# Optimization experiments

Hardware: AMD Instinct MI355X
Metric: run time of the kernel (lower is better)

## Reference

```python
import jax, jax.numpy as jnp
import numpy as np

C_IN = 256
H = W = 64
B = 2


def _conv3x3(x, w, b):
    # x: (B,C,H,W), w: (Co,Ci,3,3) -> (B,Co,H,W), stride 1, pad 1
    y = jax.lax.conv_general_dilated(x, w, (1, 1), 'SAME',
                                     dimension_numbers=('NCHW', 'OIHW', 'NCHW'))
    return y + b[None, :, None, None]


def _deform_conv3x3(x, offset, w, b):
    """torchvision-style DeformConv2d, kernel 3x3, stride 1, pad 1, dilation 1.
    x: (B,C,H,W); offset: (B,18,H,W) laid out as (k, [dy,dx]) per kernel tap;
    w: (Co,C,3,3); b: (Co,)
    """
    Bx, C, Hx, Wx = x.shape
    Co = w.shape[0]
    off = offset.reshape(Bx, 9, 2, Hx, Wx)
    # kernel tap k = ky*3 + kx, relative positions in {-1,0,1}
    ky = (jnp.arange(9) // 3 - 1).astype(x.dtype)
    kx = (jnp.arange(9) % 3 - 1).astype(x.dtype)
    py = (jnp.arange(Hx, dtype=x.dtype)[None, None, :, None]
          + ky[None, :, None, None] + off[:, :, 0])          # (B,9,H,W)
    px = (jnp.arange(Wx, dtype=x.dtype)[None, None, None, :]
          + kx[None, :, None, None] + off[:, :, 1])          # (B,9,H,W)
    y0f = jnp.floor(py)
    x0f = jnp.floor(px)
    wy = py - y0f
    wx = px - x0f
    y0 = y0f.astype(jnp.int32)
    x0 = x0f.astype(jnp.int32)
    xf = x.reshape(Bx, C, Hx * Wx)

    def corner(yc, xc, wgt):
        valid = (yc >= 0) & (yc < Hx) & (xc >= 0) & (xc < Wx)
        idx = jnp.clip(yc, 0, Hx - 1) * Wx + jnp.clip(xc, 0, Wx - 1)  # (B,9,H,W)
        g = jax.vmap(lambda xb, ib: xb[:, ib])(xf, idx.reshape(Bx, -1))  # (B,C,9HW)
        g = g.reshape(Bx, C, 9, Hx, Wx)
        return g * (wgt * valid)[:, None]  # (B,C,9,H,W)

    s = (corner(y0, x0, (1 - wy) * (1 - wx))
         + corner(y0, x0 + 1, (1 - wy) * wx)
         + corner(y0 + 1, x0, wy * (1 - wx))
         + corner(y0 + 1, x0 + 1, wy * wx))
    out = jnp.einsum('ock,bckhw->bohw', w.reshape(Co, C, 9), s)
    return out + b[None, :, None, None]


def setup_inputs() -> dict:
    key = jax.random.key(0)
    ks = jax.random.split(key, 10)
    C8 = C_IN // 8
    sc = 0.02  # small init so offsets stay O(1) pixels
    return {
        'x': jax.random.normal(ks[0], (B, C_IN, H, W), jnp.float32),
        'w_off': jax.random.normal(ks[1], (18, C_IN, 3, 3), jnp.float32) * sc,
        'b_off': jnp.zeros((18,), jnp.float32),
        'wq': jax.random.normal(ks[2], (C8, C_IN, 3, 3), jnp.float32) * sc,
        'bq': jnp.zeros((C8,), jnp.float32),
        'wk': jax.random.normal(ks[3], (C8, C_IN, 3, 3), jnp.float32) * sc,
        'bk': jnp.zeros((C8,), jnp.float32),
        'wv': jax.random.normal(ks[4], (C_IN, C_IN, 3, 3), jnp.float32) * sc,
        'bv': jnp.zeros((C_IN,), jnp.float32),
        'gamma': jnp.full((1,), 0.5, jnp.float32),  # module inits to 0; nonzero for a non-trivial baseline
    }


def reference(x, w_off, b_off, wq, bq, wk, bk, wv, bv, gamma):
    Bx, C, Hx, Wx = x.shape
    HW = Hx * Wx
    offset = _conv3x3(x, w_off, b_off)                       # (B,18,H,W)
    q = _deform_conv3x3(x, offset, wq, bq).reshape(Bx, HW, -1)  # (B,HW,C//8)
    k = _deform_conv3x3(x, offset, wk, bk).reshape(Bx, HW, -1)  # (B,HW,C//8)
    v = _deform_conv3x3(x, offset, wv, bv).reshape(Bx, HW, -1)  # (B,HW,C)
    attn = jax.nn.softmax(jnp.einsum('bqc,bkc->bqk', q, k), axis=-1)  # (B,HW,HW)
    out = jnp.einsum('bqk,bkc->bqc', attn, v).reshape(Bx, C, Hx, Wx)
    return gamma * out + x
```

## Files before the change

### kernel.cpp

```cpp
#include <hip/hip_runtime.h>
#include <math.h>
#include <stdint.h>

#define CIN 256
#define HH 64
#define WW 64
#define HW 4096
#define CHW (CIN * HW)

typedef __attribute__((ext_vector_type(8))) short short8;
typedef __attribute__((ext_vector_type(4))) float float4v;

__device__ inline unsigned short f2bf(float f) {
    union { float f; uint32_t u; } v; v.f = f;
    return (unsigned short)((v.u + 0x7FFFu + ((v.u >> 16) & 1u)) >> 16);
}
__device__ inline float bf2f(unsigned short h) {
    union { uint32_t u; float f; } v; v.u = ((uint32_t)h) << 16;
    return v.f;
}
__device__ inline uint4 ld16(const unsigned short* p) {
    uint4 r; __builtin_memcpy(&r, p, 16); return r;
}

__global__ __launch_bounds__(256) void k_offset_conv(
    const float* __restrict__ x, const float* __restrict__ w_off,
    float* __restrict__ off_part)
{
    __shared__ float red[4][64][18];
    const int bh = blockIdx.x, cg = blockIdx.y;
    const int b = bh >> 6, h = bh & 63;
    const int t = threadIdx.x;
    const int w = t & 63;
    const int wv = __builtin_amdgcn_readfirstlane(t >> 6);
    float acc[18];
#pragma unroll
    for (int i = 0; i < 18; ++i) acc[i] = 0.f;
    const float* xb = x + (size_t)b * CHW;
#pragma unroll
    for (int ci = 0; ci < 8; ++ci) {
        const int c = cg * 32 + wv * 8 + ci;
        const float* xc = xb + (size_t)c * HW;
        float r0 = (h > 0)  ? xc[(h - 1) * WW + w] : 0.f;
        float r1 =            xc[h * WW + w];
        float r2 = (h < 63) ? xc[(h + 1) * WW + w] : 0.f;
        float l0 = __shfl_up(r0, 1), l1 = __shfl_up(r1, 1), l2 = __shfl_up(r2, 1);
        float d0 = __shfl_down(r0, 1), d1 = __shfl_down(r1, 1), d2 = __shfl_down(r2, 1);
        if (w == 0)  { l0 = 0.f; l1 = 0.f; l2 = 0.f; }
        if (w == 63) { d0 = 0.f; d1 = 0.f; d2 = 0.f; }
        const float xv[9] = {l0, r0, d0, l1, r1, d1, l2, r2, d2};
        const float* wc = w_off + (size_t)c * 9;
#pragma unroll
        for (int co = 0; co < 18; ++co) {
            const float* wp = wc + (size_t)co * (CIN * 9);
#pragma unroll
            for (int k = 0; k < 9; ++k) acc[co] += wp[k] * xv[k];
        }
    }
#pragma unroll
    for (int co = 0; co < 18; ++co) red[wv][w][co] = acc[co];
    __syncthreads();
    if (t < 64) {
#pragma unroll
        for (int co = 0; co < 18; ++co) {
            float s = red[0][t][co] + red[1][t][co] + red[2][t][co] + red[3][t][co];
            off_part[((size_t)(cg * 128 + bh)) * 1152 + co * 64 + t] = s;
        }
    }
}

__global__ __launch_bounds__(256) void k_params(
    const float* __restrict__ off_part, const float* __restrict__ b_off,
    uint2* __restrict__ pbw, uint32_t* __restrict__ pba)
{
    const int bh = blockIdx.x;
    const int h = bh & 63;
    const int t = threadIdx.x;
    for (int r = 0; r < 3; ++r) {
        int sid = t + 256 * r;
        if (sid < 576) {
            int k = sid >> 6, ww = sid & 63;
            float dy = b_off[2 * k], dx = b_off[2 * k + 1];
#pragma unroll
            for (int g = 0; g < 8; ++g) {
                const float* pp = off_part + (size_t)(g * 128 + bh) * 1152;
                dy += pp[(2 * k) * 64 + ww];
                dx += pp[(2 * k + 1) * 64 + ww];
            }
            float py = (float)(h + k / 3 - 1) + dy;
            float px = (float)(ww + k % 3 - 1) + dx;
            float y0f = floorf(py), x0f = floorf(px);
            float fy = py - y0f, fx = px - x0f;
            int y0 = (int)y0f, x0 = (int)x0f;
            int yb = min(max(y0, 0), 62), xb = min(max(x0, 0), 62);
            float wr[2] = {0.f, 0.f}, wc[2] = {0.f, 0.f};
            if (y0 >= 0 && y0 < HH) wr[y0 - yb] += 1.f - fy;
            if (y0 + 1 >= 0 && y0 + 1 < HH) wr[y0 + 1 - yb] += fy;
            if (x0 >= 0 && x0 < WW) wc[x0 - xb] += 1.f - fx;
            if (x0 + 1 >= 0 && x0 + 1 < WW) wc[x0 + 1 - xb] += fx;
            uint2 pw;
            pw.x = (uint32_t)f2bf(wr[0] * wc[0]) | ((uint32_t)f2bf(wr[0] * wc[1]) << 16);
            pw.y = (uint32_t)f2bf(wr[1] * wc[0]) | ((uint32_t)f2bf(wr[1] * wc[1]) << 16);
            pbw[(size_t)bh * 576 + sid] = pw;
            pba[(size_t)bh * 576 + sid] = (uint32_t)(yb * WW + xb);
        }
    }
}

__global__ __launch_bounds__(256) void k_wcat(
    const float* __restrict__ wq, const float* __restrict__ wk, const float* __restrict__ wv_,
    const float* __restrict__ bq, const float* __restrict__ bk, const float* __restrict__ bv,
    unsigned short* __restrict__ wf, float* __restrict__ bcat)
{
    int e = (blockIdx.x * 256 + threadIdx.x) * 4;
    const float* src;
    if (e < 32 * 2304)      src = wq + e;
    else if (e < 64 * 2304) src = wk + (e - 32 * 2304);
    else                    src = wv_ + (e - 64 * 2304);
    float4 v = *(const float4*)src;
    unsigned short o[4] = {f2bf(v.x), f2bf(v.y), f2bf(v.z), f2bf(v.w)};
    int co = e / 2304;
    int k0 = e - co * 2304;
#pragma unroll
    for (int i = 0; i < 4; ++i) {
        int k = k0 + i;
        int c = (k * 7282) >> 16;
        int tap = k - c * 9;
        int kdp = tap * 256 + c;
        size_t d = ((size_t)(co >> 4) * 72 + (kdp >> 5)) * 512 + (size_t)(co & 15) * 32 + (kdp & 31);
        wf[d] = o[i];
    }
    if (blockIdx.x == 0 && threadIdx.x < 320) {
        int c = threadIdx.x;
        bcat[c] = c < 32 ? bq[c] : (c < 64 ? bk[c - 32] : bv[c - 64]);
    }
}

__global__ __launch_bounds__(256) void k_xt(
    const float* __restrict__ x, unsigned short* __restrict__ xt)
{
    __shared__ float tl[64][65];
    const int b = blockIdx.y, px0 = blockIdx.x * 64;
    const int t = threadIdx.x;
    const float* xb = x + (size_t)b * CHW;
    unsigned short* xo = xt + (size_t)b * CHW;
    for (int cb = 0; cb < 4; ++cb) {
        __syncthreads();
#pragma unroll
        for (int i = 0; i < 16; ++i) {
            int cr = (t >> 6) * 16 + i;
            tl[cr][t & 63] = xb[(size_t)(cb * 64 + cr) * HW + px0 + (t & 63)];
        }
        __syncthreads();
#pragma unroll
        for (int i = 0; i < 2; ++i) {
            int px = t >> 2;
            int sl = (t & 3) + 4 * i;
            union { uint4 v; unsigned short u[8]; } o;
#pragma unroll
            for (int j = 0; j < 8; ++j) o.u[j] = f2bf(tl[sl * 8 + j][px]);
            *(uint4*)(xo + (size_t)(px0 + px) * 256 + cb * 64 + sl * 8) = o.v;
        }
    }
}

__global__ __launch_bounds__(256) void k_dgemm(
    const unsigned short* __restrict__ xt, const uint2* __restrict__ pbw,
    const uint32_t* __restrict__ pba, const unsigned short* __restrict__ wf,
    const float* __restrict__ bcat,
    unsigned short* __restrict__ qb16, unsigned short* __restrict__ kb16,
    unsigned short* __restrict__ vb16)
{
    __shared__ uint2 prw2[144];
    __shared__ uint32_t pra2[144];
    __shared__ unsigned short tile[2][4][16][40];

    const int blk = blockIdx.x;
    const int b = blk >> 8;
    const int p0 = (blk & 255) * 16;
    const int bh = b * 64 + (p0 >> 6);
    const int w0 = p0 & 63;

    const int t = threadIdx.x;
    const int lane = t & 63;
    const int l15 = lane & 15, quad = lane >> 4;
    const int wvid = __builtin_amdgcn_readfirstlane(t >> 6);

    if (t < 144) {
        int nl9 = t / 9, tap = t - nl9 * 9;
        int src = bh * 576 + tap * 64 + w0 + nl9;
        prw2[nl9 * 9 + tap] = pbw[src];
        pra2[nl9 * 9 + tap] = pba[src];
    }

    const unsigned short* xtb = xt + (size_t)b * CHW;
    const int px = t >> 4;
    const int cl = (t >> 2) & 3;
    const int sl = t & 3;

    float4v acc[5];
#pragma unroll
    for (int s = 0; s < 5; ++s) acc[s] = (float4v){0.f, 0.f, 0.f, 0.f};

    const unsigned short* ap[5];
#pragma unroll
    for (int s = 0; s < 5; ++s)
        ap[s] = wf + (size_t)(s * 4 + wvid) * 72 * 512 + (size_t)l15 * 32 + quad * 8;

    __syncthreads();

    uint2 wcur; uint4 u00, u01, u10, u11;
    {
        int idx = px * 9 + 0;
        wcur = prw2[idx];
        const unsigned short* xp = xtb + (size_t)pra2[idx] * 256 + (0 + cl) * 32 + sl * 8;
        u00 = ld16(xp); u01 = ld16(xp + 256); u10 = ld16(xp + 16384); u11 = ld16(xp + 16640);
    }

#pragma unroll
    for (int m = 0; m < 18; ++m) {
        const int tap = m >> 1, q0 = (m & 1) * 4;

        float w00 = bf2f((unsigned short)(wcur.x & 0xFFFF));
        float w01 = bf2f((unsigned short)(wcur.x >> 16));
        float w10 = bf2f((unsigned short)(wcur.y & 0xFFFF));
        float w11 = bf2f((unsigned short)(wcur.y >> 16));
        union { uint4 v; unsigned short u[8]; } a00, a01, a10, a11, o;
        a00.v = u00; a01.v = u01; a10.v = u10; a11.v = u11;
#pragma unroll
        for (int j = 0; j < 8; ++j) {
            float v = w00 * bf2f(a00.u[j]) + w01 * bf2f(a01.u[j])
                    + w10 * bf2f(a10.u[j]) + w11 * bf2f(a11.u[j]);
            o.u[j] = f2bf(v);
        }

        if (m < 17) {
            int tapn = (m + 1) >> 1, q0n = ((m + 1) & 1) * 4;
            int idx = px * 9 + tapn;
            wcur = prw2[idx];
            const unsigned short* xp = xtb + (size_t)pra2[idx] * 256 + (q0n + cl) * 32 + sl * 8;
            u00 = ld16(xp); u01 = ld16(xp + 256); u10 = ld16(xp + 16384); u11 = ld16(xp + 16640);
        }

        *(uint4*)&tile[m & 1][cl][px][sl * 8] = o.v;
        asm volatile("s_waitcnt lgkmcnt(0)\n\ts_barrier" ::: "memory");

#pragma unroll
        for (int st = 0; st < 4; ++st) {
            const int kt = tap * 8 + q0 + st;
            short8 bfr = *(const short8*)&tile[m & 1][st][l15][quad * 8];
#pragma unroll
            for (int s = 0; s < 5; ++s) {
                uint4 a = *(const uint4*)(ap[s] + (size_t)kt * 512);
                acc[s] = __builtin_amdgcn_mfma_f32_16x16x32_bf16(*(const short8*)&a, bfr, acc[s], 0, 0, 0);
            }
        }
    }

#pragma unroll
    for (int s = 0; s < 5; ++s) {
        const int cobase = s * 64 + wvid * 16;
        unsigned short* ob; int lco; size_t nper;
        if (cobase < 32)      { ob = qb16; lco = cobase;      nper = (size_t)32 * HW; }
        else if (cobase < 64) { ob = kb16; lco = cobase - 32; nper = (size_t)32 * HW; }
        else                  { ob = vb16; lco = cobase - 64; nper = (size_t)256 * HW; }
        unsigned short* obb = ob + (size_t)b * nper;
#pragma unroll
        for (int r = 0; r < 4; ++r) {
            float val = acc[s][r] + bcat[cobase + (quad << 2) + r];
            obb[(size_t)(lco + (quad << 2) + r) * HW + p0 + l15] = f2bf(val);
        }
    }
}

__global__ __launch_bounds__(256) void k_vtrans(
    const unsigned short* __restrict__ vb16, unsigned short* __restrict__ vb16T)
{
    const int jt = blockIdx.x, b = blockIdx.y;
    const int cc = threadIdx.x;
    const unsigned short* src = vb16 + (size_t)b * CHW + (size_t)(jt * 64) * 256 + cc;
    unsigned short* dst = vb16T + (size_t)b * CHW + (size_t)cc * 4096 + jt * 64;
#pragma unroll
    for (int o = 0; o < 8; ++o) {
        union { uint4 v; unsigned short u[8]; } tmp;
#pragma unroll
        for (int j = 0; j < 8; ++j) tmp.u[j] = src[(o * 8 + j) * 256];
        *(uint4*)(dst + o * 8) = tmp.v;
    }
}

#define SM_SHIFT 16.0f
__global__ __launch_bounds__(256) void k_attn(
    const unsigned short* __restrict__ qb16, const unsigned short* __restrict__ kb16,
    const unsigned short* __restrict__ vt, const float* __restrict__ x,
    const float* __restrict__ gamma, float* __restrict__ out)
{
    __shared__ unsigned short ptl[4][16 * 40];
    __shared__ unsigned short Vt[2][64][40];
    __shared__ unsigned short Kt[2][32][36];
    __shared__ float red[2][64][20];

    const int qt = blockIdx.x, ch = blockIdx.y, b = blockIdx.z;
    const int t = threadIdx.x;
    const int lane = t & 63;
    const int wv = t >> 6;
    const int g = wv & 1, jh = wv >> 1;
    const int l15 = lane & 15, quad = lane >> 4;
    const int cc0 = ch * 64;

    const unsigned short* Qb = qb16 + (size_t)b * (32 * 4096);
    const unsigned short* Kb = kb16 + (size_t)b * (32 * 4096);
    const unsigned short* VT = vt + (size_t)b * CHW;

    const int q0 = qt * 32 + g * 16;
    short8 qfr = *(const short8*)(Qb + (size_t)(q0 + l15) * 32 + quad * 8);

    const int vcc = t >> 2, voff = (t & 3) * 8;
    const int ktile = t >> 7, ktl = t & 127;
    const int krow = ktl >> 2, koff = (ktl & 3) * 8;

    float l_i = 0.f;
    float4v acc[4];
#pragma unroll
    for (int s = 0; s < 4; ++s) acc[s] = (float4v){0.f, 0.f, 0.f, 0.f};
    unsigned short* pw = ptl[wv];

    for (int rnd = 0; rnd < 64; ++rnd) {
        const int j0a = rnd * 32;
        uint4 v0 = *(const uint4*)(VT + (size_t)(cc0 + vcc) * 4096 + j0a + voff);
        uint4 v1 = *(const uint4*)(VT + (size_t)(cc0 + vcc) * 4096 + 2048 + j0a + voff);
        uint4 kv = *(const uint4*)(Kb + (size_t)(ktile * 2048 + j0a + krow) * 32 + koff);
        __syncthreads();
        *(uint4*)&Vt[0][vcc][voff] = v0;
        *(uint4*)&Vt[1][vcc][voff] = v1;
        *(uint4*)&Kt[ktile][krow][koff] = kv;
        __syncthreads();
        short8 kfr0 = *(const short8*)&Kt[jh][l15][quad * 8];
        short8 kfr1 = *(const short8*)&Kt[jh][16 + l15][quad * 8];
        float4v s0 = (float4v){0.f, 0.f, 0.f, 0.f}, s1 = s0;
        s0 = __builtin_amdgcn_mfma_f32_16x16x32_bf16(kfr0, qfr, s0, 0, 0, 0);
        s1 = __builtin_amdgcn_mfma_f32_16x16x32_bf16(kfr1, qfr, s1, 0, 0, 0);
        float p[8]; float ls = 0.f;
#pragma unroll
        for (int r = 0; r < 4; ++r) { p[r] = __expf(s0[r] - SM_SHIFT); ls += p[r]; }
#pragma unroll
        for (int r = 0; r < 4; ++r) { p[4 + r] = __expf(s1[r] - SM_SHIFT); ls += p[4 + r]; }
        l_i += ls;
        union { uint2 v; unsigned short u[4]; } pk0, pk1;
#pragma unroll
        for (int r = 0; r < 4; ++r) { pk0.u[r] = f2bf(p[r]); pk1.u[r] = f2bf(p[4 + r]); }
        *(uint2*)&pw[l15 * 40 + (quad << 2)] = pk0.v;
        *(uint2*)&pw[l15 * 40 + 16 + (quad << 2)] = pk1.v;
        short8 pfr = *(const short8*)&pw[l15 * 40 + quad * 8];
#pragma unroll
        for (int s = 0; s < 4; ++s) {
            short8 vfr = *(const short8*)&Vt[jh][s * 16 + l15][quad * 8];
            acc[s] = __builtin_amdgcn_mfma_f32_16x16x32_bf16(pfr, vfr, acc[s], 0, 0, 0);
        }
    }

    l_i += __shfl_xor(l_i, 16);
    l_i += __shfl_xor(l_i, 32);

    __syncthreads();
    if (jh == 1) {
#pragma unroll
        for (int s = 0; s < 4; ++s) *(float4v*)&red[g][lane][s * 4] = acc[s];
        red[g][lane][16] = l_i;
    }
    __syncthreads();
    if (jh == 0) {
#pragma unroll
        for (int s = 0; s < 4; ++s) {
            float4v o = *(const float4v*)&red[g][lane][s * 4];
            acc[s][0] += o[0]; acc[s][1] += o[1]; acc[s][2] += o[2]; acc[s][3] += o[3];
        }
        l_i += red[g][lane][16];
        float lr[4];
#pragma unroll
        for (int r = 0; r < 4; ++r) lr[r] = __shfl(l_i, (quad << 2) + r);
        const float gm = gamma[0];
        const float* xb = x + (size_t)b * CHW;
        float* ob = out + (size_t)b * CHW;
#pragma unroll
        for (int s = 0; s < 4; ++s) {
#pragma unroll
            for (int r = 0; r < 4; ++r) {
                int q = q0 + (quad << 2) + r;
                int cc = cc0 + s * 16 + l15;
                size_t idx = (size_t)q * 256 + cc;
                ob[idx] = gm * (acc[s][r] / lr[r]) + xb[idx];
            }
        }
    }
}

extern "C" void kernel_launch(void* const* d_in, const int* in_sizes, int n_in,
                              void* d_out, int out_size, void* d_ws, size_t ws_size,
                              hipStream_t stream)
{
    (void)in_sizes; (void)n_in; (void)out_size; (void)ws_size;
    const float* x     = (const float*)d_in[0];
    const float* w_off = (const float*)d_in[1];
    const float* b_off = (const float*)d_in[2];
    const float* wq    = (const float*)d_in[3];
    const float* bq    = (const float*)d_in[4];
    const float* wk    = (const float*)d_in[5];
    const float* bk    = (const float*)d_in[6];
    const float* wv    = (const float*)d_in[7];
    const float* bv    = (const float*)d_in[8];
    const float* gamma = (const float*)d_in[9];
    float* out = (float*)d_out;

    char* ws = (char*)d_ws;
    uint2*          pbw     = (uint2*)(ws + 589824);
    uint32_t*       pba     = (uint32_t*)(ws + 1179648);
    unsigned short* qb16    = (unsigned short*)(ws + 1474560);
    unsigned short* kb16    = (unsigned short*)(ws + 1998848);
    unsigned short* vb16T   = (unsigned short*)(ws + 2523136);
    unsigned short* wfb     = (unsigned short*)(ws + 6717440);
    float*          bcat    = (float*)(ws + 8192000);
    float*          off_part = (float*)d_out;
    unsigned short* vb16     = (unsigned short*)d_out;
    unsigned short* xtb      = (unsigned short*)((char*)d_out + 4194304);

    k_offset_conv<<<dim3(128, 8), 256, 0, stream>>>(x, w_off, off_part);
    k_params<<<dim3(128), 256, 0, stream>>>(off_part, b_off, pbw, pba);
    k_wcat<<<dim3(720), 256, 0, stream>>>(wq, wk, wv, bq, bk, bv, wfb, bcat);
    k_xt<<<dim3(64, 2), 256, 0, stream>>>(x, xtb);
    k_dgemm<<<dim3(512), 256, 0, stream>>>(xtb, pbw, pba, wfb, bcat, qb16, kb16, vb16);
    k_vtrans<<<dim3(64, 2), 256, 0, stream>>>(vb16, vb16T);
    k_attn<<<dim3(128, 4, 2), 256, 0, stream>>>(qb16, kb16, vb16T, x, gamma, out);
}
```

Measured before the change: 260.7 us.

## Double queries per attention block and prefetch next K/V tile into registers

```diff
diff --git a/kernel.cpp b/kernel.cpp
--- a/kernel.cpp
+++ b/kernel.cpp
@@ -295,10 +295,10 @@
     const unsigned short* __restrict__ vt, const float* __restrict__ x,
     const float* __restrict__ gamma, float* __restrict__ out)
 {
-    __shared__ unsigned short ptl[4][16 * 40];
-    __shared__ unsigned short Vt[2][64][40];
+    __shared__ unsigned short ptl[8][16 * 40];
+    __shared__ unsigned short Vt[2][64][36];
     __shared__ unsigned short Kt[2][32][36];
-    __shared__ float red[2][64][20];
+    __shared__ float red[2][64][36];
 
     const int qt = blockIdx.x, ch = blockIdx.y, b = blockIdx.z;
     const int t = threadIdx.x;
@@ -312,84 +312,131 @@
     const unsigned short* Kb = kb16 + (size_t)b * (32 * 4096);
     const unsigned short* VT = vt + (size_t)b * CHW;
 
-    const int q0 = qt * 32 + g * 16;
-    short8 qfr = *(const short8*)(Qb + (size_t)(q0 + l15) * 32 + quad * 8);
+    const int qbase = qt * 64 + g * 32;
+    short8 qfr0 = *(const short8*)(Qb + (size_t)(qbase + l15) * 32 + quad * 8);
+    short8 qfr1 = *(const short8*)(Qb + (size_t)(qbase + 16 + l15) * 32 + quad * 8);
 
     const int vcc = t >> 2, voff = (t & 3) * 8;
     const int ktile = t >> 7, ktl = t & 127;
     const int krow = ktl >> 2, koff = (ktl & 3) * 8;
 
-    float l_i = 0.f;
-    float4v acc[4];
-#pragma unroll
-    for (int s = 0; s < 4; ++s) acc[s] = (float4v){0.f, 0.f, 0.f, 0.f};
-    unsigned short* pw = ptl[wv];
+    float l_i0 = 0.f, l_i1 = 0.f;
+    float4v acc[2][4];
+#pragma unroll
+    for (int u = 0; u < 2; ++u)
+#pragma unroll
+        for (int s = 0; s < 4; ++s) acc[u][s] = (float4v){0.f, 0.f, 0.f, 0.f};
+    unsigned short* pw0 = ptl[wv * 2];
+    unsigned short* pw1 = ptl[wv * 2 + 1];
+
+    uint4 v0, v1, kv;
+    {
+        const unsigned short* vp = VT + (size_t)(cc0 + vcc) * 4096 + voff;
+        v0 = ld16(vp);
+        v1 = ld16(vp + 2048);
+        kv = ld16(Kb + (size_t)(ktile * 2048 + krow) * 32 + koff);
+    }
 
     for (int rnd = 0; rnd < 64; ++rnd) {
-        const int j0a = rnd * 32;
-        uint4 v0 = *(const uint4*)(VT + (size_t)(cc0 + vcc) * 4096 + j0a + voff);
-        uint4 v1 = *(const uint4*)(VT + (size_t)(cc0 + vcc) * 4096 + 2048 + j0a + voff);
-        uint4 kv = *(const uint4*)(Kb + (size_t)(ktile * 2048 + j0a + krow) * 32 + koff);
-        __syncthreads();
+        asm volatile("s_waitcnt lgkmcnt(0)\n\ts_barrier" ::: "memory");
         *(uint4*)&Vt[0][vcc][voff] = v0;
         *(uint4*)&Vt[1][vcc][voff] = v1;
         *(uint4*)&Kt[ktile][krow][koff] = kv;
-        __syncthreads();
+        asm volatile("s_waitcnt lgkmcnt(0)\n\ts_barrier" ::: "memory");
+
+        if (rnd < 63) {
+            const int j0n = (rnd + 1) * 32;
+            const unsigned short* vp = VT + (size_t)(cc0 + vcc) * 4096 + j0n + voff;
+            v0 = ld16(vp);
+            v1 = ld16(vp + 2048);
+            kv = ld16(Kb + (size_t)(ktile * 2048 + j0n + krow) * 32 + koff);
+        }
+
         short8 kfr0 = *(const short8*)&Kt[jh][l15][quad * 8];
         short8 kfr1 = *(const short8*)&Kt[jh][16 + l15][quad * 8];
-        float4v s0 = (float4v){0.f, 0.f, 0.f, 0.f}, s1 = s0;
-        s0 = __builtin_amdgcn_mfma_f32_16x16x32_bf16(kfr0, qfr, s0, 0, 0, 0);
-        s1 = __builtin_amdgcn_mfma_f32_16x16x32_bf16(kfr1, qfr, s1, 0, 0, 0);
-        float p[8]; float ls = 0.f;
-#pragma unroll
-        for (int r = 0; r < 4; ++r) { p[r] = __expf(s0[r] - SM_SHIFT); ls += p[r]; }
-#pragma unroll
-        for (int r = 0; r < 4; ++r) { p[4 + r] = __expf(s1[r] - SM_SHIFT); ls += p[4 + r]; }
-        l_i += ls;
-        union { uint2 v; unsigned short u[4]; } pk0, pk1;
-#pragma unroll
-        for (int r = 0; r < 4; ++r) { pk0.u[r] = f2bf(p[r]); pk1.u[r] = f2bf(p[4 + r]); }
-        *(uint2*)&pw[l15 * 40 + (quad << 2)] = pk0.v;
-        *(uint2*)&pw[l15 * 40 + 16 + (quad << 2)] = pk1.v;
-        short8 pfr = *(const short8*)&pw[l15 * 40 + quad * 8];
+        float4v s0 = (float4v){0.f, 0.f, 0.f, 0.f}, s1 = s0, s2 = s0, s3 = s0;
+        s0 = __builtin_amdgcn_mfma_f32_16x16x32_bf16(kfr0, qfr0, s0, 0, 0, 0);
+        s1 = __builtin_amdgcn_mfma_f32_16x16x32_bf16(kfr1, qfr0, s1, 0, 0, 0);
+        s2 = __builtin_amdgcn_mfma_f32_16x16x32_bf16(kfr0, qfr1, s2, 0, 0, 0);
+        s3 = __builtin_amdgcn_mfma_f32_16x16x32_bf16(kfr1, qfr1, s3, 0, 0, 0);
+
+        float p[16]; float ls0 = 0.f, ls1 = 0.f;
+#pragma unroll
+        for (int r = 0; r < 4; ++r) { p[r]      = __expf(s0[r] - SM_SHIFT); ls0 += p[r]; }
+#pragma unroll
+        for (int r = 0; r < 4; ++r) { p[4 + r]  = __expf(s1[r] - SM_SHIFT); ls0 += p[4 + r]; }
+#pragma unroll
+        for (int r = 0; r < 4; ++r) { p[8 + r]  = __expf(s2[r] - SM_SHIFT); ls1 += p[8 + r]; }
+#pragma unroll
+        for (int r = 0; r < 4; ++r) { p[12 + r] = __expf(s3[r] - SM_SHIFT); ls1 += p[12 + r]; }
+        l_i0 += ls0; l_i1 += ls1;
+
+        union { uint2 v; unsigned short u[4]; } pk0, pk1, pk2, pk3;
+#pragma unroll
+        for (int r = 0; r < 4; ++r) {
+            pk0.u[r] = f2bf(p[r]);      pk1.u[r] = f2bf(p[4 + r]);
+            pk2.u[r] = f2bf(p[8 + r]);  pk3.u[r] = f2bf(p[12 + r]);
+        }
+        *(uint2*)&pw0[l15 * 40 + (quad << 2)]      = pk0.v;
+        *(uint2*)&pw0[l15 * 40 + 16 + (quad << 2)] = pk1.v;
+        *(uint2*)&pw1[l15 * 40 + (quad << 2)]      = pk2.v;
+        *(uint2*)&pw1[l15 * 40 + 16 + (quad << 2)] = pk3.v;
+        short8 pfr0 = *(const short8*)&pw0[l15 * 40 + quad * 8];
+        short8 pfr1 = *(const short8*)&pw1[l15 * 40 + quad * 8];
+
 #pragma unroll
         for (int s = 0; s < 4; ++s) {
             short8 vfr = *(const short8*)&Vt[jh][s * 16 + l15][quad * 8];
-            acc[s] = __builtin_amdgcn_mfma_f32_16x16x32_bf16(pfr, vfr, acc[s], 0, 0, 0);
-        }
-    }
-
-    l_i += __shfl_xor(l_i, 16);
-    l_i += __shfl_xor(l_i, 32);
+            acc[0][s] = __builtin_amdgcn_mfma_f32_16x16x32_bf16(pfr0, vfr, acc[0][s], 0, 0, 0);
+            acc[1][s] = __builtin_amdgcn_mfma_f32_16x16x32_bf16(pfr1, vfr, acc[1][s], 0, 0, 0);
+        }
+    }
+
+    l_i0 += __shfl_xor(l_i0, 16); l_i0 += __shfl_xor(l_i0, 32);
+    l_i1 += __shfl_xor(l_i1, 16); l_i1 += __shfl_xor(l_i1, 32);
 
     __syncthreads();
     if (jh == 1) {
 #pragma unroll
-        for (int s = 0; s < 4; ++s) *(float4v*)&red[g][lane][s * 4] = acc[s];
-        red[g][lane][16] = l_i;
+        for (int u = 0; u < 2; ++u)
+#pragma unroll
+            for (int s = 0; s < 4; ++s) *(float4v*)&red[g][lane][u * 16 + s * 4] = acc[u][s];
+        red[g][lane][32] = l_i0;
+        red[g][lane][33] = l_i1;
     }
     __syncthreads();
     if (jh == 0) {
 #pragma unroll
-        for (int s = 0; s < 4; ++s) {
-            float4v o = *(const float4v*)&red[g][lane][s * 4];
-            acc[s][0] += o[0]; acc[s][1] += o[1]; acc[s][2] += o[2]; acc[s][3] += o[3];
-        }
-        l_i += red[g][lane][16];
-        float lr[4];
-#pragma unroll
-        for (int r = 0; r < 4; ++r) lr[r] = __shfl(l_i, (quad << 2) + r);
+        for (int u = 0; u < 2; ++u)
+#pragma unroll
+            for (int s = 0; s < 4; ++s) {
+                float4v o = *(const float4v*)&red[g][lane][u * 16 + s * 4];
+                acc[u][s][0] += o[0]; acc[u][s][1] += o[1];
+                acc[u][s][2] += o[2]; acc[u][s][3] += o[3];
+            }
+        l_i0 += red[g][lane][32];
+        l_i1 += red[g][lane][33];
+        float lr0[4], lr1[4];
+#pragma unroll
+        for (int r = 0; r < 4; ++r) {
+            lr0[r] = __shfl(l_i0, (quad << 2) + r);
+            lr1[r] = __shfl(l_i1, (quad << 2) + r);
+        }
         const float gm = gamma[0];
         const float* xb = x + (size_t)b * CHW;
         float* ob = out + (size_t)b * CHW;
 #pragma unroll
-        for (int s = 0; s < 4; ++s) {
-#pragma unroll
-            for (int r = 0; r < 4; ++r) {
-                int q = q0 + (quad << 2) + r;
-                int cc = cc0 + s * 16 + l15;
-                size_t idx = (size_t)q * 256 + cc;
-                ob[idx] = gm * (acc[s][r] / lr[r]) + xb[idx];
+        for (int u = 0; u < 2; ++u) {
+#pragma unroll
+            for (int s = 0; s < 4; ++s) {
+#pragma unroll
+                for (int r = 0; r < 4; ++r) {
+                    int q = qbase + u * 16 + (quad << 2) + r;
+                    int cc = cc0 + s * 16 + l15;
+                    size_t idx = (size_t)q * 256 + cc;
+                    float lr = u ? lr1[r] : lr0[r];
+                    ob[idx] = gm * (acc[u][s][r] / lr) + xb[idx];
+                }
             }
         }
     }
@@ -430,5 +477,5 @@
     k_xt<<<dim3(64, 2), 256, 0, stream>>>(x, xtb);
     k_dgemm<<<dim3(512), 256, 0, stream>>>(xtb, pbw, pba, wfb, bcat, qb16, kb16, vb16);
     k_vtrans<<<dim3(64, 2), 256, 0, stream>>>(vb16, vb16T);
-    k_attn<<<dim3(128, 4, 2), 256, 0, stream>>>(qb16, kb16, vb16T, x, gamma, out);
-}
+    k_attn<<<dim3(64, 4, 2), 256, 0, stream>>>(qb16, kb16, vb16T, x, gamma, out);
+}
```

Result: no change. 262.8 us (+0.8%).

## Prefetch next K/V tile in attention loop and use packed bf16 conversion

Applied to the files above, without the earlier changes.

```diff
diff --git a/kernel.cpp b/kernel.cpp
--- a/kernel.cpp
+++ b/kernel.cpp
@@ -21,6 +21,11 @@
 }
 __device__ inline uint4 ld16(const unsigned short* p) {
     uint4 r; __builtin_memcpy(&r, p, 16); return r;
+}
+__device__ inline uint32_t cvtpk(float lo, float hi) {
+    uint32_t r;
+    asm("v_cvt_pk_bf16_f32 %0, %1, %2" : "=v"(r) : "v"(lo), "v"(hi));
+    return r;
 }
 
 __global__ __launch_bounds__(256) void k_offset_conv(
@@ -225,14 +230,17 @@
         float w01 = bf2f((unsigned short)(wcur.x >> 16));
         float w10 = bf2f((unsigned short)(wcur.y & 0xFFFF));
         float w11 = bf2f((unsigned short)(wcur.y >> 16));
-        union { uint4 v; unsigned short u[8]; } a00, a01, a10, a11, o;
+        union { uint4 v; unsigned short u[8]; } a00, a01, a10, a11;
         a00.v = u00; a01.v = u01; a10.v = u10; a11.v = u11;
+        float vv[8];
 #pragma unroll
         for (int j = 0; j < 8; ++j) {
-            float v = w00 * bf2f(a00.u[j]) + w01 * bf2f(a01.u[j])
-                    + w10 * bf2f(a10.u[j]) + w11 * bf2f(a11.u[j]);
-            o.u[j] = f2bf(v);
-        }
+            vv[j] = w00 * bf2f(a00.u[j]) + w01 * bf2f(a01.u[j])
+                  + w10 * bf2f(a10.u[j]) + w11 * bf2f(a11.u[j]);
+        }
+        uint4 ov;
+        ov.x = cvtpk(vv[0], vv[1]); ov.y = cvtpk(vv[2], vv[3]);
+        ov.z = cvtpk(vv[4], vv[5]); ov.w = cvtpk(vv[6], vv[7]);
 
         if (m < 17) {
             int tapn = (m + 1) >> 1, q0n = ((m + 1) & 1) * 4;
@@ -242,7 +250,7 @@
             u00 = ld16(xp); u01 = ld16(xp + 256); u10 = ld16(xp + 16384); u11 = ld16(xp + 16640);
         }
 
-        *(uint4*)&tile[m & 1][cl][px][sl * 8] = o.v;
+        *(uint4*)&tile[m & 1][cl][px][sl * 8] = ov;
         asm volatile("s_waitcnt lgkmcnt(0)\n\ts_barrier" ::: "memory");
 
 #pragma unroll
@@ -290,13 +298,14 @@
 }
 
 #define SM_SHIFT 16.0f
+#define LOG2E 1.4426950408889634f
 __global__ __launch_bounds__(256) void k_attn(
     const unsigned short* __restrict__ qb16, const unsigned short* __restrict__ kb16,
     const unsigned short* __restrict__ vt, const float* __restrict__ x,
     const float* __restrict__ gamma, float* __restrict__ out)
 {
-    __shared__ unsigned short ptl[4][16 * 40];
-    __shared__ unsigned short Vt[2][64][40];
+    __shared__ unsigned short ptl[4][16 * 36];
+    __shared__ unsigned short Vt[2][64][36];
     __shared__ unsigned short Kt[2][32][36];
     __shared__ float red[2][64][20];
 
@@ -325,16 +334,29 @@
     for (int s = 0; s < 4; ++s) acc[s] = (float4v){0.f, 0.f, 0.f, 0.f};
     unsigned short* pw = ptl[wv];
 
+    uint4 v0, v1, kv;
+    {
+        const unsigned short* vp = VT + (size_t)(cc0 + vcc) * 4096 + voff;
+        v0 = ld16(vp);
+        v1 = ld16(vp + 2048);
+        kv = ld16(Kb + (size_t)(ktile * 2048 + krow) * 32 + koff);
+    }
+
     for (int rnd = 0; rnd < 64; ++rnd) {
-        const int j0a = rnd * 32;
-        uint4 v0 = *(const uint4*)(VT + (size_t)(cc0 + vcc) * 4096 + j0a + voff);
-        uint4 v1 = *(const uint4*)(VT + (size_t)(cc0 + vcc) * 4096 + 2048 + j0a + voff);
-        uint4 kv = *(const uint4*)(Kb + (size_t)(ktile * 2048 + j0a + krow) * 32 + koff);
-        __syncthreads();
+        asm volatile("s_waitcnt lgkmcnt(0)\n\ts_barrier" ::: "memory");
         *(uint4*)&Vt[0][vcc][voff] = v0;
         *(uint4*)&Vt[1][vcc][voff] = v1;
         *(uint4*)&Kt[ktile][krow][koff] = kv;
-        __syncthreads();
+        asm volatile("s_waitcnt lgkmcnt(0)\n\ts_barrier" ::: "memory");
+
+        if (rnd < 63) {
+            const int j0n = (rnd + 1) * 32;
+            const unsigned short* vp = VT + (size_t)(cc0 + vcc) * 4096 + j0n + voff;
+            v0 = ld16(vp);
+            v1 = ld16(vp + 2048);
+            kv = ld16(Kb + (size_t)(ktile * 2048 + j0n + krow) * 32 + koff);
+        }
+
         short8 kfr0 = *(const short8*)&Kt[jh][l15][quad * 8];
         short8 kfr1 = *(const short8*)&Kt[jh][16 + l15][quad * 8];
         float4v s0 = (float4v){0.f, 0.f, 0.f, 0.f}, s1 = s0;
@@ -342,16 +364,20 @@
         s1 = __builtin_amdgcn_mfma_f32_16x16x32_bf16(kfr1, qfr, s1, 0, 0, 0);
         float p[8]; float ls = 0.f;
 #pragma unroll
-        for (int r = 0; r < 4; ++r) { p[r] = __expf(s0[r] - SM_SHIFT); ls += p[r]; }
-#pragma unroll
-        for (int r = 0; r < 4; ++r) { p[4 + r] = __expf(s1[r] - SM_SHIFT); ls += p[4 + r]; }
+        for (int r = 0; r < 4; ++r) {
+            p[r] = exp2f(__builtin_fmaf(s0[r], LOG2E, -SM_SHIFT * LOG2E)); ls += p[r];
+        }
+#pragma unroll
+        for (int r = 0; r < 4; ++r) {
+            p[4 + r] = exp2f(__builtin_fmaf(s1[r], LOG2E, -SM_SHIFT * LOG2E)); ls += p[4 + r];
+        }
         l_i += ls;
-        union { uint2 v; unsigned short u[4]; } pk0, pk1;
-#pragma unroll
-        for (int r = 0; r < 4; ++r) { pk0.u[r] = f2bf(p[r]); pk1.u[r] = f2bf(p[4 + r]); }
-        *(uint2*)&pw[l15 * 40 + (quad << 2)] = pk0.v;
-        *(uint2*)&pw[l15 * 40 + 16 + (quad << 2)] = pk1.v;
-        short8 pfr = *(const short8*)&pw[l15 * 40 + quad * 8];
+        uint2 pk0, pk1;
+        pk0.x = cvtpk(p[0], p[1]); pk0.y = cvtpk(p[2], p[3]);
+        pk1.x = cvtpk(p[4], p[5]); pk1.y = cvtpk(p[6], p[7]);
+        *(uint2*)&pw[l15 * 36 + (quad << 2)] = pk0;
+        *(uint2*)&pw[l15 * 36 + 16 + (quad << 2)] = pk1;
+        short8 pfr = *(const short8*)&pw[l15 * 36 + quad * 8];
 #pragma unroll
         for (int s = 0; s < 4; ++s) {
             short8 vfr = *(const short8*)&Vt[jh][s * 16 + l15][quad * 8];
```

New measurement: 290.7 us. 11.5% more time.
